# Performance work log

Measured on AMD Instinct MI355X. Metric: run time of the kernel, lower is better.

The kernel has to match this reference:

```python
import jax, jax.numpy as jnp
import numpy as np

T, B, E, H, L, V = 35, 128, 200, 512, 2, 10000


def setup_inputs() -> dict:
    key = jax.random.key(0)
    ks = jax.random.split(key, 8)
    s = 0.05  # weight init scale
    return {
        "inputs": jax.random.randint(ks[0], (T, B), 0, V),
        "hidden": jnp.zeros((L, B, H), jnp.float32),
        "emb": jax.random.normal(ks[1], (V, E), jnp.float32) * s,
        "Wx0": jax.random.normal(ks[2], (3, H, E), jnp.float32) * s,
        "Wx": jax.random.normal(ks[3], (L - 1, 3, H, H), jnp.float32) * s,
        "Wh": jax.random.normal(ks[4], (L, 3, H, H), jnp.float32) * s,
        "bh": jax.random.normal(ks[5], (L, 3, H), jnp.float32) * s,
        "Wout": jax.random.normal(ks[6], (V, H), jnp.float32) * s,
        "bout": jnp.zeros((V,), jnp.float32),
    }


def reference(inputs, hidden, emb, Wx0, Wx, Wh, bh, Wout, bout):
    # inputs: [T,B] int; hidden: [L,B,H]
    x = emb[inputs]  # [T,B,E]
    num_layers = hidden.shape[0]

    def step(h_prev, x_t):
        data = x_t  # dropout is identity (keep_prob=1.0)
        new_h = []
        for j in range(num_layers):
            Wxj = Wx0 if j == 0 else Wx[j - 1]
            gx = jnp.einsum('bi,ghi->gbh', data, Wxj)  # [3,B,H], no bias on x-side
            hp = h_prev[j]
            reset = jax.nn.sigmoid(gx[0] + hp @ Wh[j, 0].T + bh[j, 0])
            forget = jax.nn.sigmoid(gx[1] + hp @ Wh[j, 1].T + bh[j, 1])
            tild = jnp.tanh(gx[2] + (reset * hp) @ Wh[j, 2].T + bh[j, 2])
            hn = (1.0 - forget) * hp + forget * tild
            new_h.append(hn)
            data = hn  # dropout identity
        logit = data @ Wout.T + bout  # [B,V]
        return jnp.stack(new_h), logit

    h_final, logits = jax.lax.scan(step, hidden, x)
    return logits, h_final
```

## Files before the change

kernel.cpp:

```cpp
#include <hip/hip_runtime.h>
#include <hip/hip_bf16.h>

#define T_ 35
#define B_ 128
#define E_ 200
#define H_ 512
#define L_ 2
#define V_ 10000
#define BH_ (B_ * H_)
#define KPAD 224
#define NCL 4
#define CLW 48
#define NWG (NCL * CLW)

typedef __attribute__((ext_vector_type(8))) short bf16x8;
typedef __attribute__((ext_vector_type(4))) float f32x4;

__device__ __forceinline__ unsigned short f2bf(float f) {
    union { float f; unsigned u; } c; c.f = f;
    unsigned r = c.u + 0x7FFF + ((c.u >> 16) & 1);
    return (unsigned short)(r >> 16);
}
__device__ __forceinline__ float bf2f(unsigned short u) {
    union { unsigned u; float f; } c; c.u = ((unsigned)u) << 16; return c.f;
}

__device__ __forceinline__ bf16x8 cvt8(const float* src) {
    float4 w0 = *(const float4*)src;
    float4 w1 = *(const float4*)(src + 4);
    bf16x8 v;
    v[0] = (short)f2bf(w0.x); v[1] = (short)f2bf(w0.y);
    v[2] = (short)f2bf(w0.z); v[3] = (short)f2bf(w0.w);
    v[4] = (short)f2bf(w1.x); v[5] = (short)f2bf(w1.y);
    v[6] = (short)f2bf(w1.z); v[7] = (short)f2bf(w1.w);
    return v;
}

__device__ __forceinline__ void store_pair_bf16(unsigned short* buf, int idx,
                                                float v, int lane) {
    float vn = __shfl_xor(v, 1);
    if ((lane & 1) == 0) {
        unsigned p = (unsigned)f2bf(v) | ((unsigned)f2bf(vn) << 16);
        __hip_atomic_store((unsigned*)(buf + idx), p,
                           __ATOMIC_RELAXED, __HIP_MEMORY_SCOPE_AGENT);
    }
}

__global__ void prep_all(const float* __restrict__ emb, const float* __restrict__ Wx0,
                         const float* __restrict__ hidden, const float* __restrict__ Wout,
                         unsigned short* embB, unsigned short* wx0cat,
                         unsigned short* WoutB,
                         unsigned short* h0bt, unsigned short* h1bfx, int* flags) {
    int job = blockIdx.y;
    int stride = gridDim.x * blockDim.x;
    int i0 = blockIdx.x * blockDim.x + threadIdx.x;
    if (job == 0) {
        for (int i = i0; i < V_ * KPAD; i += stride) {
            int v = i / KPAD, k = i - v * KPAD;
            embB[i] = (k < E_) ? f2bf(emb[v * E_ + k]) : (unsigned short)0;
        }
    } else if (job == 1) {
        for (int i = i0; i < 1536 * KPAD; i += stride) {
            int n = i / KPAD, k = i - n * KPAD;
            wx0cat[i] = (k < E_) ? f2bf(Wx0[n * E_ + k]) : (unsigned short)0;
        }
    } else if (job == 2) {
        for (int i = i0; i < 2 * BH_; i += stride) {
            if (i < BH_) h0bt[i] = f2bf(hidden[i]);
            else         h1bfx[i - BH_] = f2bf(hidden[i]);
        }
        for (int i = i0; i < NWG * 32; i += stride) flags[i] = 0;
    } else {
        for (int i = i0; i < V_ * H_; i += stride) WoutB[i] = f2bf(Wout[i]);
    }
}

__global__ __launch_bounds__(256) void xside_gemm(
    const int* __restrict__ inputs, const unsigned short* __restrict__ embB,
    const unsigned short* __restrict__ wx0cat, float* __restrict__ gx0) {
    int m0 = blockIdx.x * 128, n0 = blockIdx.y * 128;
    int wave = threadIdx.x >> 6, lane = threadIdx.x & 63;
    int wr = wave >> 1, wc = wave & 1;
    int am = m0 + wr * 64, bn = n0 + wc * 64;
    int lr = lane & 15, lk = (lane >> 4) * 8;

    f32x4 acc[4][4] = {};
    int id[4];
    #pragma unroll
    for (int i = 0; i < 4; ++i) id[i] = inputs[am + i * 16 + lr];

    for (int k0 = 0; k0 < KPAD; k0 += 32) {
        bf16x8 a[4], b[4];
        #pragma unroll
        for (int i = 0; i < 4; ++i)
            a[i] = *(const bf16x8*)(embB + (size_t)id[i] * KPAD + k0 + lk);
        #pragma unroll
        for (int j = 0; j < 4; ++j)
            b[j] = *(const bf16x8*)(wx0cat + (size_t)(bn + j * 16 + lr) * KPAD + k0 + lk);
        #pragma unroll
        for (int i = 0; i < 4; ++i)
            #pragma unroll
            for (int j = 0; j < 4; ++j)
                acc[i][j] = __builtin_amdgcn_mfma_f32_16x16x32_bf16(a[i], b[j], acc[i][j], 0, 0, 0);
    }
    int crow0 = (lane >> 4) * 4, ccol = lane & 15;
    #pragma unroll
    for (int i = 0; i < 4; ++i) {
        #pragma unroll
        for (int r = 0; r < 4; ++r) {
            int row = am + i * 16 + crow0 + r;
            int t = row >> 7, b = row & 127;
            #pragma unroll
            for (int j = 0; j < 4; ++j) {
                int col = bn + j * 16 + ccol;
                int g = col >> 9, h = col & 511;
                gx0[((size_t)(t * 3 + g) * 128 + b) * 512 + h] = acc[i][j][r];
            }
        }
    }
}

__device__ __forceinline__ void cl_bar(int* flb, int wgl, int gen) {
    __syncthreads();
    if (threadIdx.x == 0)
        __hip_atomic_store(flb + wgl * 32, gen,
                           __ATOMIC_RELAXED, __HIP_MEMORY_SCOPE_AGENT);
    if (threadIdx.x < CLW) {
        while (__hip_atomic_load(flb + threadIdx.x * 32, __ATOMIC_RELAXED,
                                 __HIP_MEMORY_SCOPE_AGENT) < gen)
            __builtin_amdgcn_s_sleep(1);
    }
    __syncthreads();
}

__global__ __launch_bounds__(512) void scan_kernel(
    const float* __restrict__ gx0,
    const float* __restrict__ Wx, const float* __restrict__ Wh,
    const float* __restrict__ bh, const float* __restrict__ hidden,
    unsigned short* h0bt, unsigned short* rh0t, unsigned short* rh1t,
    unsigned short* h1bfx, int* flags, float* hfinal_out) {
    __shared__ unsigned short wlds[96 * 512];

    const int tid = threadIdx.x;
    const int bx = blockIdx.x;
    const int cl = bx & 3;
    const int wgl = bx >> 2;
    const int lane = tid & 63;
    const int wave = tid >> 6;
    const int lr = lane & 15;
    const int hi = lane >> 4;
    const int lk8 = hi * 8;
    const int ccol = lane & 15;
    const int crow0 = hi * 4;
    const int R0 = cl * 32;

    const bool isL0 = (wgl < 16);
    const int wid = wgl - 16;
    int* flb = flags + cl * CLW * 32;

    if (isL0) {
        for (int i = tid; i < 96 * 64; i += 512) {
            int lc = i >> 6, kg = i & 63;
            int g = lc >> 5, h = (wgl << 5) + (lc & 31);
            const float* src = Wh + (size_t)(g * 512 + h) * 512 + kg * 8;
            *(bf16x8*)(wlds + lc * 512 + (kg ^ (lc & 7)) * 8) = cvt8(src);
        }
    } else {
        for (int i = tid; i < 48 * 128; i += 512) {
            int lc = i >> 7, kg = i & 127;
            int g = lc >> 4, h = (wid << 4) + (lc & 15);
            const float* src = (kg < 64)
                ? Wx + (size_t)(g * 512 + h) * 512 + kg * 8
                : Wh + (size_t)(3 * 512 * 512) + (size_t)(g * 512 + h) * 512 + (kg - 64) * 8;
            *(bf16x8*)(wlds + lc * 1024 + (kg ^ (lc & 7)) * 8) = cvt8(src);
        }
    }

    const int mt0 = wave >> 2, nt0 = wave & 3;
    const int mt1 = (wave >> 1) & 1, nt1 = wave & 1;
    float h0reg[4], freg0[4], bias_p1_0 = 0.f, bias_p2_0 = 0.f;
    float h1reg[4], freg1[4], bias_p1_1 = 0.f, bias_p2_1 = 0.f;
    bf16x8 a0keep[16];

    if (isL0) {
        const int base = wgl << 5;
        int g = nt0 >> 1;
        int hp1 = base + (nt0 & 1) * 16 + ccol;
        bias_p1_0 = bh[g * 512 + hp1];
        if (nt0 >= 2) {
            int hc = base + (nt0 - 2) * 16 + ccol;
            int rowg = R0 + mt0 * 16;
            #pragma unroll
            for (int r = 0; r < 4; ++r)
                h0reg[r] = hidden[(size_t)(rowg + crow0 + r) * 512 + hc];
            bias_p2_0 = bh[1024 + hc];
        }
    } else {
        const int base = wid << 4;
        int hc = base + ccol;
        if (wave < 4) {
            bias_p1_1 = bh[1536 + nt1 * 512 + hc];
            if (nt1 == 1) {
                int rowg = R0 + mt1 * 16;
                #pragma unroll
                for (int r = 0; r < 4; ++r)
                    h1reg[r] = hidden[(size_t)BH_ + (size_t)(rowg + crow0 + r) * 512 + hc];
                bias_p2_1 = bh[2560 + hc];
            }
        }
    }
    __syncthreads();

    for (int s = 0; s <= 2 * T_ + 1; ++s) {
        int t = s >> 1;
        if ((s & 1) == 0) {
            if (isL0) {
                if (t < T_) {
                    const int base = wgl << 5;
                    const int rowg = R0 + mt0 * 16;
                    const unsigned short* hprev = h0bt + (size_t)t * BH_;
                    unsigned short* rh0 = rh0t + (size_t)t * BH_;
                    bf16x8 a[16];
                    #pragma unroll
                    for (int ks = 0; ks < 16; ++ks)
                        a[ks] = *(const bf16x8*)(hprev + (size_t)(rowg + lr) * 512 + ks * 32 + lk8);
                    int g = nt0 >> 1;
                    int h = base + (nt0 & 1) * 16 + ccol;
                    float gxv[4];
                    {
                        const float* gx = gx0 + (size_t)(t * 3 + g) * BH_ + h;
                        #pragma unroll
                        for (int r = 0; r < 4; ++r)
                            gxv[r] = gx[(rowg + crow0 + r) * 512];
                    }
                    f32x4 acc = {0.f, 0.f, 0.f, 0.f};
                    #pragma unroll
                    for (int ks = 0; ks < 16; ++ks) {
                        int kg = 4 * ks + hi;
                        int c = nt0 * 16 + lr;
                        bf16x8 b = *(const bf16x8*)(wlds + c * 512 + (kg ^ (c & 7)) * 8);
                        acc = __builtin_amdgcn_mfma_f32_16x16x32_bf16(a[ks], b, acc, 0, 0, 0);
                    }
                    #pragma unroll
                    for (int r = 0; r < 4; ++r) {
                        int b = rowg + crow0 + r;
                        float v = acc[r] + gxv[r] + bias_p1_0;
                        float sg = 1.f / (1.f + __expf(-v));
                        if (nt0 < 2) {
                            float h0p = bf2f(hprev[(size_t)b * 512 + h]);
                            store_pair_bf16(rh0, b * 512 + h, sg * h0p, lane);
                        } else {
                            freg0[r] = sg;
                        }
                    }
                }
            } else {
                int tc = t - 1;
                if (tc >= 0 && tc < T_ && wave < 4) {
                    const int base = wid << 4;
                    const int rowg = R0 + mt1 * 16;
                    const unsigned short* h0cur = h0bt + (size_t)(tc + 1) * BH_;
                    const unsigned short* h1prev = h1bfx + (size_t)tc * BH_;
                    unsigned short* rh1 = rh1t + (size_t)tc * BH_;
                    bf16x8 a1[16];
                    #pragma unroll
                    for (int ks = 0; ks < 16; ++ks) {
                        a0keep[ks] = *(const bf16x8*)(h0cur + (size_t)(rowg + lr) * 512 + ks * 32 + lk8);
                        a1[ks] = *(const bf16x8*)(h1prev + (size_t)(rowg + lr) * 512 + ks * 32 + lk8);
                    }
                    f32x4 acc = {0.f, 0.f, 0.f, 0.f};
                    #pragma unroll
                    for (int ks = 0; ks < 16; ++ks) {
                        int kg = 4 * ks + hi;
                        int c = nt1 * 16 + lr;
                        bf16x8 b = *(const bf16x8*)(wlds + c * 1024 + (kg ^ (c & 7)) * 8);
                        acc = __builtin_amdgcn_mfma_f32_16x16x32_bf16(a0keep[ks], b, acc, 0, 0, 0);
                    }
                    #pragma unroll
                    for (int ks = 0; ks < 16; ++ks) {
                        int kg = 64 + 4 * ks + hi;
                        int c = nt1 * 16 + lr;
                        bf16x8 b = *(const bf16x8*)(wlds + c * 1024 + (kg ^ (c & 7)) * 8);
                        acc = __builtin_amdgcn_mfma_f32_16x16x32_bf16(a1[ks], b, acc, 0, 0, 0);
                    }
                    int h = base + ccol;
                    #pragma unroll
                    for (int r = 0; r < 4; ++r) {
                        int b = rowg + crow0 + r;
                        float v = acc[r] + bias_p1_1;
                        float sg = 1.f / (1.f + __expf(-v));
                        if (nt1 == 0) {
                            float h1p = bf2f(h1prev[(size_t)b * 512 + h]);
                            store_pair_bf16(rh1, b * 512 + h, sg * h1p, lane);
                        } else {
                            freg1[r] = sg;
                        }
                    }
                }
            }
        } else {
            if (isL0) {
                if (t < T_ && nt0 >= 2) {
                    const int base = wgl << 5;
                    const int ntp = nt0 - 2;
                    const int rowg = R0 + mt0 * 16;
                    const unsigned short* rh0 = rh0t + (size_t)t * BH_;
                    unsigned short* h0nx = h0bt + (size_t)(t + 1) * BH_;
                    bf16x8 a[16];
                    #pragma unroll
                    for (int ks = 0; ks < 16; ++ks)
                        a[ks] = *(const bf16x8*)(rh0 + (size_t)(rowg + lr) * 512 + ks * 32 + lk8);
                    int h = base + ntp * 16 + ccol;
                    float gxv[4];
                    {
                        const float* gx = gx0 + (size_t)(t * 3 + 2) * BH_ + h;
                        #pragma unroll
                        for (int r = 0; r < 4; ++r)
                            gxv[r] = gx[(rowg + crow0 + r) * 512];
                    }
                    f32x4 acc = {0.f, 0.f, 0.f, 0.f};
                    #pragma unroll
                    for (int ks = 0; ks < 16; ++ks) {
                        int kg = 4 * ks + hi;
                        int c = 64 + ntp * 16 + lr;
                        bf16x8 b = *(const bf16x8*)(wlds + c * 512 + (kg ^ (c & 7)) * 8);
                        acc = __builtin_amdgcn_mfma_f32_16x16x32_bf16(a[ks], b, acc, 0, 0, 0);
                    }
                    #pragma unroll
                    for (int r = 0; r < 4; ++r) {
                        int b = rowg + crow0 + r;
                        float v = acc[r] + gxv[r] + bias_p2_0;
                        float tld = tanhf(v);
                        float hn = h0reg[r] + freg0[r] * (tld - h0reg[r]);
                        h0reg[r] = hn;
                        store_pair_bf16(h0nx, b * 512 + h, hn, lane);
                    }
                }
            } else {
                int tc = t - 1;
                if (tc >= 0 && tc < T_ && wave < 4 && nt1 == 1) {
                    const int base = wid << 4;
                    const int rowg = R0 + mt1 * 16;
                    const unsigned short* rh1 = rh1t + (size_t)tc * BH_;
                    unsigned short* h1nx = h1bfx + (size_t)(tc + 1) * BH_;
                    bf16x8 a1[16];
                    #pragma unroll
                    for (int ks = 0; ks < 16; ++ks)
                        a1[ks] = *(const bf16x8*)(rh1 + (size_t)(rowg + lr) * 512 + ks * 32 + lk8);
                    f32x4 acc = {0.f, 0.f, 0.f, 0.f};
                    #pragma unroll
                    for (int ks = 0; ks < 16; ++ks) {
                        int kg = 4 * ks + hi;
                        int c = 32 + lr;
                        bf16x8 b = *(const bf16x8*)(wlds + c * 1024 + (kg ^ (c & 7)) * 8);
                        acc = __builtin_amdgcn_mfma_f32_16x16x32_bf16(a0keep[ks], b, acc, 0, 0, 0);
                    }
                    #pragma unroll
                    for (int ks = 0; ks < 16; ++ks) {
                        int kg = 64 + 4 * ks + hi;
                        int c = 32 + lr;
                        bf16x8 b = *(const bf16x8*)(wlds + c * 1024 + (kg ^ (c & 7)) * 8);
                        acc = __builtin_amdgcn_mfma_f32_16x16x32_bf16(a1[ks], b, acc, 0, 0, 0);
                    }
                    int h = base + ccol;
                    #pragma unroll
                    for (int r = 0; r < 4; ++r) {
                        int b = rowg + crow0 + r;
                        float v = acc[r] + bias_p2_1;
                        float tld = tanhf(v);
                        float hn = h1reg[r] + freg1[r] * (tld - h1reg[r]);
                        h1reg[r] = hn;
                        store_pair_bf16(h1nx, b * 512 + h, hn, lane);
                    }
                }
            }
        }
        cl_bar(flb, wgl, s + 1);
    }

    if (isL0) {
        if (nt0 >= 2) {
            const int base = wgl << 5;
            int hc = base + (nt0 - 2) * 16 + ccol;
            int rowg = R0 + mt0 * 16;
            #pragma unroll
            for (int r = 0; r < 4; ++r)
                hfinal_out[(size_t)(rowg + crow0 + r) * 512 + hc] = h0reg[r];
        }
    } else if (wave < 4 && nt1 == 1) {
        const int base = wid << 4;
        int rowg = R0 + mt1 * 16;
        #pragma unroll
        for (int r = 0; r < 4; ++r)
            hfinal_out[(size_t)BH_ + (size_t)(rowg + crow0 + r) * 512 + base + ccol] = h1reg[r];
    }
}

#define MT_ (T_ * B_ / 128)
#define NT_ ((V_ + 127) / 128)
__global__ __launch_bounds__(256) void logits_gemm(
    const unsigned short* __restrict__ A, const unsigned short* __restrict__ Bw,
    const float* __restrict__ bout, float* __restrict__ C) {
    const int nwg = MT_ * NT_;
    const int q = nwg / 8, rr = nwg % 8;
    int bid = blockIdx.x;
    int xcd = bid % 8, idx = bid / 8;
    int wgid = (xcd < rr ? xcd * (q + 1) : rr * (q + 1) + (xcd - rr) * q) + idx;
    int n0 = (wgid / MT_) * 128;
    int m0 = (wgid % MT_) * 128;

    int wave = threadIdx.x >> 6, lane = threadIdx.x & 63;
    int wr = wave >> 1, wc = wave & 1;
    int am = m0 + wr * 64, bn = n0 + wc * 64;
    int lr = lane & 15, lk = (lane >> 4) * 8;

    f32x4 acc[4][4] = {};
    bf16x8 a[4], b[4], an[4], bnx[4];
    #pragma unroll
    for (int i = 0; i < 4; ++i)
        a[i] = *(const bf16x8*)(A + (size_t)(am + i * 16 + lr) * H_ + lk);
    #pragma unroll
    for (int j = 0; j < 4; ++j) {
        int colc = bn + j * 16 + lr; if (colc >= V_) colc = V_ - 1;
        b[j] = *(const bf16x8*)(Bw + (size_t)colc * H_ + lk);
    }
    for (int k0 = 0; k0 < H_; k0 += 32) {
        if (k0 + 32 < H_) {
            #pragma unroll
            for (int i = 0; i < 4; ++i)
                an[i] = *(const bf16x8*)(A + (size_t)(am + i * 16 + lr) * H_ + k0 + 32 + lk);
            #pragma unroll
            for (int j = 0; j < 4; ++j) {
                int colc = bn + j * 16 + lr; if (colc >= V_) colc = V_ - 1;
                bnx[j] = *(const bf16x8*)(Bw + (size_t)colc * H_ + k0 + 32 + lk);
            }
        }
        #pragma unroll
        for (int i = 0; i < 4; ++i)
            #pragma unroll
            for (int j = 0; j < 4; ++j)
                acc[i][j] = __builtin_amdgcn_mfma_f32_16x16x32_bf16(a[i], b[j], acc[i][j], 0, 0, 0);
        #pragma unroll
        for (int i = 0; i < 4; ++i) { a[i] = an[i]; b[i] = bnx[i]; }
    }
    int crow0 = (lane >> 4) * 4, ccol = lane & 15;
    #pragma unroll
    for (int j = 0; j < 4; ++j) {
        int col = bn + j * 16 + ccol;
        if (col >= V_) continue;
        float bv = bout[col];
        #pragma unroll
        for (int i = 0; i < 4; ++i) {
            #pragma unroll
            for (int r = 0; r < 4; ++r) {
                int row = am + i * 16 + crow0 + r;
                __builtin_nontemporal_store(acc[i][j][r] + bv, &C[(size_t)row * V_ + col]);
            }
        }
    }
}

extern "C" void kernel_launch(void* const* d_in, const int* in_sizes, int n_in,
                              void* d_out, int out_size, void* d_ws, size_t ws_size,
                              hipStream_t stream) {
    const int*   inputs = (const int*)  d_in[0];
    const float* hidden = (const float*)d_in[1];
    const float* emb    = (const float*)d_in[2];
    const float* Wx0    = (const float*)d_in[3];
    const float* Wx     = (const float*)d_in[4];
    const float* Wh     = (const float*)d_in[5];
    const float* bh     = (const float*)d_in[6];
    const float* Wout   = (const float*)d_in[7];
    const float* bout   = (const float*)d_in[8];
    float* out = (float*)d_out;
    (void)in_sizes; (void)n_in; (void)out_size; (void)ws_size;

    char* ws = (char*)d_ws;
    size_t off = 0;
    auto alloc = [&](size_t bytes) -> void* {
        void* p = ws + off;
        off += (bytes + 255) & ~(size_t)255;
        return p;
    };
    unsigned short* embB   = (unsigned short*)alloc((size_t)V_ * KPAD * 2);
    unsigned short* wx0cat = (unsigned short*)alloc((size_t)1536 * KPAD * 2);
    unsigned short* WoutB  = (unsigned short*)alloc((size_t)V_ * H_ * 2);
    unsigned short* h1bfx  = (unsigned short*)alloc((size_t)(T_ + 1) * BH_ * 2);
    int* flags = (int*)alloc(NWG * 32 * 4);

    float* gx0 = out;
    unsigned short* scr = (unsigned short*)(out + (size_t)T_ * 3 * BH_);
    unsigned short* h0bt = scr;
    unsigned short* rh0t = scr + (size_t)(T_ + 1) * BH_;
    unsigned short* rh1t = scr + (size_t)(2 * T_ + 1) * BH_;

    prep_all<<<dim3(1024, 4), dim3(256), 0, stream>>>(
        emb, Wx0, hidden, Wout, embB, wx0cat, WoutB, h0bt, h1bfx, flags);
    xside_gemm<<<dim3(T_, 12), dim3(256), 0, stream>>>(inputs, embB, wx0cat, gx0);
    scan_kernel<<<dim3(NWG), dim3(512), 0, stream>>>(
        gx0, Wx, Wh, bh, hidden,
        h0bt, rh0t, rh1t, h1bfx, flags,
        out + (size_t)T_ * B_ * V_);
    logits_gemm<<<dim3(MT_ * NT_), dim3(256), 0, stream>>>(
        h1bfx + BH_, WoutB, bout, out);
}
```

Measured before the change: 653.0 us.

## Split cluster barrier into separate layer-0 and layer-1 barriers with dependency flags

Replaces the single 48-workgroup cluster barrier with separate barriers for layer-0 (16 WGs) and layer-1 (32 WGs). Layer-1 waits only on the layer-0 progress flags it depends on, so layer 0 can run ahead and the two layers are no longer in lockstep. MFMA accumulation is also split into two independent accumulator chains to shorten dependency latency. The risk is relaxed ordering on the flag protocol and layer 0 racing ahead. Correctness depends on the flag generations matching.

```diff
diff --git a/kernel.cpp b/kernel.cpp
--- a/kernel.cpp
+++ b/kernel.cpp
@@ -120,14 +120,31 @@
     }
 }
 
-__device__ __forceinline__ void cl_bar(int* flb, int wgl, int gen) {
+__device__ __forceinline__ void bar_l0(int* flb, int wgl, int gen) {
     __syncthreads();
     if (threadIdx.x == 0)
         __hip_atomic_store(flb + wgl * 32, gen,
                            __ATOMIC_RELAXED, __HIP_MEMORY_SCOPE_AGENT);
-    if (threadIdx.x < CLW) {
+    if (threadIdx.x < 16) {
         while (__hip_atomic_load(flb + threadIdx.x * 32, __ATOMIC_RELAXED,
                                  __HIP_MEMORY_SCOPE_AGENT) < gen)
+            __builtin_amdgcn_s_sleep(1);
+    }
+    __syncthreads();
+}
+
+__device__ __forceinline__ void bar_l1(int* flb, int wid, int gen, int l0need) {
+    __syncthreads();
+    if (threadIdx.x == 0)
+        __hip_atomic_store(flb + (16 + wid) * 32, gen,
+                           __ATOMIC_RELAXED, __HIP_MEMORY_SCOPE_AGENT);
+    if (threadIdx.x < 32) {
+        while (__hip_atomic_load(flb + (16 + threadIdx.x) * 32, __ATOMIC_RELAXED,
+                                 __HIP_MEMORY_SCOPE_AGENT) < gen)
+            __builtin_amdgcn_s_sleep(1);
+    } else if (threadIdx.x < 48) {
+        while (__hip_atomic_load(flb + (threadIdx.x - 32) * 32, __ATOMIC_RELAXED,
+                                 __HIP_MEMORY_SCOPE_AGENT) < l0need)
             __builtin_amdgcn_s_sleep(1);
     }
     __syncthreads();
@@ -211,52 +228,108 @@
     }
     __syncthreads();
 
-    for (int s = 0; s <= 2 * T_ + 1; ++s) {
-        int t = s >> 1;
-        if ((s & 1) == 0) {
-            if (isL0) {
-                if (t < T_) {
-                    const int base = wgl << 5;
-                    const int rowg = R0 + mt0 * 16;
-                    const unsigned short* hprev = h0bt + (size_t)t * BH_;
-                    unsigned short* rh0 = rh0t + (size_t)t * BH_;
-                    bf16x8 a[16];
-                    #pragma unroll
-                    for (int ks = 0; ks < 16; ++ks)
-                        a[ks] = *(const bf16x8*)(hprev + (size_t)(rowg + lr) * 512 + ks * 32 + lk8);
-                    int g = nt0 >> 1;
-                    int h = base + (nt0 & 1) * 16 + ccol;
-                    float gxv[4];
-                    {
-                        const float* gx = gx0 + (size_t)(t * 3 + g) * BH_ + h;
-                        #pragma unroll
-                        for (int r = 0; r < 4; ++r)
-                            gxv[r] = gx[(rowg + crow0 + r) * 512];
-                    }
-                    f32x4 acc = {0.f, 0.f, 0.f, 0.f};
-                    #pragma unroll
-                    for (int ks = 0; ks < 16; ++ks) {
-                        int kg = 4 * ks + hi;
-                        int c = nt0 * 16 + lr;
-                        bf16x8 b = *(const bf16x8*)(wlds + c * 512 + (kg ^ (c & 7)) * 8);
-                        acc = __builtin_amdgcn_mfma_f32_16x16x32_bf16(a[ks], b, acc, 0, 0, 0);
-                    }
-                    #pragma unroll
-                    for (int r = 0; r < 4; ++r) {
-                        int b = rowg + crow0 + r;
-                        float v = acc[r] + gxv[r] + bias_p1_0;
-                        float sg = 1.f / (1.f + __expf(-v));
-                        if (nt0 < 2) {
-                            float h0p = bf2f(hprev[(size_t)b * 512 + h]);
-                            store_pair_bf16(rh0, b * 512 + h, sg * h0p, lane);
-                        } else {
-                            freg0[r] = sg;
-                        }
-                    }
-                }
-            } else {
-                int tc = t - 1;
-                if (tc >= 0 && tc < T_ && wave < 4) {
+    if (isL0) {
+        for (int s = 0; s < 2 * T_; ++s) {
+            bar_l0(flb, wgl, s);
+            int t = s >> 1;
+            if ((s & 1) == 0) {
+                const int base = wgl << 5;
+                const int rowg = R0 + mt0 * 16;
+                const unsigned short* hprev = h0bt + (size_t)t * BH_;
+                unsigned short* rh0 = rh0t + (size_t)t * BH_;
+                bf16x8 a[16];
+                #pragma unroll
+                for (int ks = 0; ks < 16; ++ks)
+                    a[ks] = *(const bf16x8*)(hprev + (size_t)(rowg + lr) * 512 + ks * 32 + lk8);
+                int g = nt0 >> 1;
+                int h = base + (nt0 & 1) * 16 + ccol;
+                float gxv[4];
+                {
+                    const float* gx = gx0 + (size_t)(t * 3 + g) * BH_ + h;
+                    #pragma unroll
+                    for (int r = 0; r < 4; ++r)
+                        gxv[r] = gx[(rowg + crow0 + r) * 512];
+                }
+                f32x4 accA = {0.f, 0.f, 0.f, 0.f}, accB = {0.f, 0.f, 0.f, 0.f};
+                #pragma unroll
+                for (int ks = 0; ks < 16; ks += 2) {
+                    int c = nt0 * 16 + lr;
+                    int kgA = 4 * ks + hi, kgB = 4 * (ks + 1) + hi;
+                    bf16x8 bA = *(const bf16x8*)(wlds + c * 512 + (kgA ^ (c & 7)) * 8);
+                    bf16x8 bB = *(const bf16x8*)(wlds + c * 512 + (kgB ^ (c & 7)) * 8);
+                    accA = __builtin_amdgcn_mfma_f32_16x16x32_bf16(a[ks], bA, accA, 0, 0, 0);
+                    accB = __builtin_amdgcn_mfma_f32_16x16x32_bf16(a[ks + 1], bB, accB, 0, 0, 0);
+                }
+                #pragma unroll
+                for (int r = 0; r < 4; ++r) {
+                    int b = rowg + crow0 + r;
+                    float v = accA[r] + accB[r] + gxv[r] + bias_p1_0;
+                    float sg = 1.f / (1.f + __expf(-v));
+                    if (nt0 < 2) {
+                        float h0p = bf2f(hprev[(size_t)b * 512 + h]);
+                        store_pair_bf16(rh0, b * 512 + h, sg * h0p, lane);
+                    } else {
+                        freg0[r] = sg;
+                    }
+                }
+            } else if (nt0 >= 2) {
+                const int base = wgl << 5;
+                const int ntp = nt0 - 2;
+                const int rowg = R0 + mt0 * 16;
+                const unsigned short* rh0 = rh0t + (size_t)t * BH_;
+                unsigned short* h0nx = h0bt + (size_t)(t + 1) * BH_;
+                bf16x8 a[16];
+                #pragma unroll
+                for (int ks = 0; ks < 16; ++ks)
+                    a[ks] = *(const bf16x8*)(rh0 + (size_t)(rowg + lr) * 512 + ks * 32 + lk8);
+                int h = base + ntp * 16 + ccol;
+                float gxv[4];
+                {
+                    const float* gx = gx0 + (size_t)(t * 3 + 2) * BH_ + h;
+                    #pragma unroll
+                    for (int r = 0; r < 4; ++r)
+                        gxv[r] = gx[(rowg + crow0 + r) * 512];
+                }
+                f32x4 accA = {0.f, 0.f, 0.f, 0.f}, accB = {0.f, 0.f, 0.f, 0.f};
+                #pragma unroll
+                for (int ks = 0; ks < 16; ks += 2) {
+                    int c = 64 + ntp * 16 + lr;
+                    int kgA = 4 * ks + hi, kgB = 4 * (ks + 1) + hi;
+                    bf16x8 bA = *(const bf16x8*)(wlds + c * 512 + (kgA ^ (c & 7)) * 8);
+                    bf16x8 bB = *(const bf16x8*)(wlds + c * 512 + (kgB ^ (c & 7)) * 8);
+                    accA = __builtin_amdgcn_mfma_f32_16x16x32_bf16(a[ks], bA, accA, 0, 0, 0);
+                    accB = __builtin_amdgcn_mfma_f32_16x16x32_bf16(a[ks + 1], bB, accB, 0, 0, 0);
+                }
+                #pragma unroll
+                for (int r = 0; r < 4; ++r) {
+                    int b = rowg + crow0 + r;
+                    float v = accA[r] + accB[r] + gxv[r] + bias_p2_0;
+                    float tld = tanhf(v);
+                    float hn = h0reg[r] + freg0[r] * (tld - h0reg[r]);
+                    h0reg[r] = hn;
+                    store_pair_bf16(h0nx, b * 512 + h, hn, lane);
+                }
+            }
+        }
+        __syncthreads();
+        if (tid == 0)
+            __hip_atomic_store(flb + wgl * 32, 2 * T_,
+                               __ATOMIC_RELAXED, __HIP_MEMORY_SCOPE_AGENT);
+        if (nt0 >= 2) {
+            const int base = wgl << 5;
+            int hc = base + (nt0 - 2) * 16 + ccol;
+            int rowg = R0 + mt0 * 16;
+            #pragma unroll
+            for (int r = 0; r < 4; ++r)
+                hfinal_out[(size_t)(rowg + crow0 + r) * 512 + hc] = h0reg[r];
+        }
+    } else {
+        for (int s = 0; s < 2 * T_; ++s) {
+            int tc = s >> 1;
+            int l0need = ((s & 1) == 0) ? (2 * tc + 2) : 0;
+            bar_l1(flb, wid, s, l0need);
+            if ((s & 1) == 0) {
+                if (wave < 4) {
                     const int base = wid << 4;
                     const int rowg = R0 + mt1 * 16;
                     const unsigned short* h0cur = h0bt + (size_t)(tc + 1) * BH_;
@@ -268,26 +341,26 @@
                         a0keep[ks] = *(const bf16x8*)(h0cur + (size_t)(rowg + lr) * 512 + ks * 32 + lk8);
                         a1[ks] = *(const bf16x8*)(h1prev + (size_t)(rowg + lr) * 512 + ks * 32 + lk8);
                     }
-                    f32x4 acc = {0.f, 0.f, 0.f, 0.f};
+                    f32x4 accA = {0.f, 0.f, 0.f, 0.f}, accB = {0.f, 0.f, 0.f, 0.f};
                     #pragma unroll
                     for (int ks = 0; ks < 16; ++ks) {
                         int kg = 4 * ks + hi;
                         int c = nt1 * 16 + lr;
                         bf16x8 b = *(const bf16x8*)(wlds + c * 1024 + (kg ^ (c & 7)) * 8);
-                        acc = __builtin_amdgcn_mfma_f32_16x16x32_bf16(a0keep[ks], b, acc, 0, 0, 0);
+                        accA = __builtin_amdgcn_mfma_f32_16x16x32_bf16(a0keep[ks], b, accA, 0, 0, 0);
                     }
                     #pragma unroll
                     for (int ks = 0; ks < 16; ++ks) {
                         int kg = 64 + 4 * ks + hi;
                         int c = nt1 * 16 + lr;
                         bf16x8 b = *(const bf16x8*)(wlds + c * 1024 + (kg ^ (c & 7)) * 8);
-                        acc = __builtin_amdgcn_mfma_f32_16x16x32_bf16(a1[ks], b, acc, 0, 0, 0);
+                        accB = __builtin_amdgcn_mfma_f32_16x16x32_bf16(a1[ks], b, accB, 0, 0, 0);
                     }
                     int h = base + ccol;
                     #pragma unroll
                     for (int r = 0; r < 4; ++r) {
                         int b = rowg + crow0 + r;
-                        float v = acc[r] + bias_p1_1;
+                        float v = accA[r] + accB[r] + bias_p1_1;
                         float sg = 1.f / (1.f + __expf(-v));
                         if (nt1 == 0) {
                             float h1p = bf2f(h1prev[(size_t)b * 512 + h]);
@@ -297,48 +370,8 @@
                         }
                     }
                 }
-            }
-        } else {
-            if (isL0) {
-                if (t < T_ && nt0 >= 2) {
-                    const int base = wgl << 5;
-                    const int ntp = nt0 - 2;
-                    const int rowg = R0 + mt0 * 16;
-                    const unsigned short* rh0 = rh0t + (size_t)t * BH_;
-                    unsigned short* h0nx = h0bt + (size_t)(t + 1) * BH_;
-                    bf16x8 a[16];
-                    #pragma unroll
-                    for (int ks = 0; ks < 16; ++ks)
-                        a[ks] = *(const bf16x8*)(rh0 + (size_t)(rowg + lr) * 512 + ks * 32 + lk8);
-                    int h = base + ntp * 16 + ccol;
-                    float gxv[4];
-                    {
-                        const float* gx = gx0 + (size_t)(t * 3 + 2) * BH_ + h;
-                        #pragma unroll
-                        for (int r = 0; r < 4; ++r)
-                            gxv[r] = gx[(rowg + crow0 + r) * 512];
-                    }
-                    f32x4 acc = {0.f, 0.f, 0.f, 0.f};
-                    #pragma unroll
-                    for (int ks = 0; ks < 16; ++ks) {
-                        int kg = 4 * ks + hi;
-                        int c = 64 + ntp * 16 + lr;
-                        bf16x8 b = *(const bf16x8*)(wlds + c * 512 + (kg ^ (c & 7)) * 8);
-                        acc = __builtin_amdgcn_mfma_f32_16x16x32_bf16(a[ks], b, acc, 0, 0, 0);
-                    }
-                    #pragma unroll
-                    for (int r = 0; r < 4; ++r) {
-                        int b = rowg + crow0 + r;
-                        float v = acc[r] + gxv[r] + bias_p2_0;
-                        float tld = tanhf(v);
-                        float hn = h0reg[r] + freg0[r] * (tld - h0reg[r]);
-                        h0reg[r] = hn;
-                        store_pair_bf16(h0nx, b * 512 + h, hn, lane);
-                    }
-                }
             } else {
-                int tc = t - 1;
-                if (tc >= 0 && tc < T_ && wave < 4 && nt1 == 1) {
+                if (wave < 4 && nt1 == 1) {
                     const int base = wid << 4;
                     const int rowg = R0 + mt1 * 16;
                     const unsigned short* rh1 = rh1t + (size_t)tc * BH_;
@@ -347,26 +380,26 @@
                     #pragma unroll
                     for (int ks = 0; ks < 16; ++ks)
                         a1[ks] = *(const bf16x8*)(rh1 + (size_t)(rowg + lr) * 512 + ks * 32 + lk8);
-                    f32x4 acc = {0.f, 0.f, 0.f, 0.f};
+                    f32x4 accA = {0.f, 0.f, 0.f, 0.f}, accB = {0.f, 0.f, 0.f, 0.f};
                     #pragma unroll
                     for (int ks = 0; ks < 16; ++ks) {
                         int kg = 4 * ks + hi;
                         int c = 32 + lr;
                         bf16x8 b = *(const bf16x8*)(wlds + c * 1024 + (kg ^ (c & 7)) * 8);
-                        acc = __builtin_amdgcn_mfma_f32_16x16x32_bf16(a0keep[ks], b, acc, 0, 0, 0);
+                        accA = __builtin_amdgcn_mfma_f32_16x16x32_bf16(a0keep[ks], b, accA, 0, 0, 0);
                     }
                     #pragma unroll
                     for (int ks = 0; ks < 16; ++ks) {
                         int kg = 64 + 4 * ks + hi;
                         int c = 32 + lr;
                         bf16x8 b = *(const bf16x8*)(wlds + c * 1024 + (kg ^ (c & 7)) * 8);
-                        acc = __builtin_amdgcn_mfma_f32_16x16x32_bf16(a1[ks], b, acc, 0, 0, 0);
+                        accB = __builtin_amdgcn_mfma_f32_16x16x32_bf16(a1[ks], b, accB, 0, 0, 0);
                     }
                     int h = base + ccol;
                     #pragma unroll
                     for (int r = 0; r < 4; ++r) {
                         int b = rowg + crow0 + r;
-                        float v = acc[r] + bias_p2_1;
+                        float v = accA[r] + accB[r] + bias_p2_1;
                         float tld = tanhf(v);
                         float hn = h1reg[r] + freg1[r] * (tld - h1reg[r]);
                         h1reg[r] = hn;
@@ -375,24 +408,13 @@
                 }
             }
         }
-        cl_bar(flb, wgl, s + 1);
-    }
-
-    if (isL0) {
-        if (nt0 >= 2) {
-            const int base = wgl << 5;
-            int hc = base + (nt0 - 2) * 16 + ccol;
-            int rowg = R0 + mt0 * 16;
+        if (wave < 4 && nt1 == 1) {
+            const int base = wid << 4;
+            int rowg = R0 + mt1 * 16;
             #pragma unroll
             for (int r = 0; r < 4; ++r)
-                hfinal_out[(size_t)(rowg + crow0 + r) * 512 + hc] = h0reg[r];
-        }
-    } else if (wave < 4 && nt1 == 1) {
-        const int base = wid << 4;
-        int rowg = R0 + mt1 * 16;
-        #pragma unroll
-        for (int r = 0; r < 4; ++r)
-            hfinal_out[(size_t)BH_ + (size_t)(rowg + crow0 + r) * 512 + base + ccol] = h1reg[r];
+                hfinal_out[(size_t)BH_ + (size_t)(rowg + crow0 + r) * 512 + base + ccol] = h1reg[r];
+        }
     }
 }
 
```

New measurement: 602.6 us. -7.7%, faster.

## Decouple GRU layer workgroups with per-phase counters and split-K across all waves

Applied to the files above, without the earlier changes.

Replaces the lockstep per-cluster flag barrier, where all 48 workgroups wait for each other every phase, with separate per-phase atomic counters for layer 0 and layer 1. Layer 1 now polls only the layer-0 counter it depends on, so the two layers pipeline rather than run in a fixed skewed lockstep. It also splits the K dimension of the candidate and layer-1 matmuls across otherwise idle waves, reducing partial sums through LDS, so all 8 waves do work and each wave's serial MFMA chain is shorter. The cost is extra __syncthreads and LDS traffic per phase and a larger counter array. Layer 0 may also run ahead of layer 1 with no backpressure, which depends on every timestep keeping its own buffers.

```diff
diff --git a/kernel.cpp b/kernel.cpp
--- a/kernel.cpp
+++ b/kernel.cpp
@@ -12,6 +12,7 @@
 #define NCL 4
 #define CLW 48
 #define NWG (NCL * CLW)
+#define NPH 80
 
 typedef __attribute__((ext_vector_type(8))) short bf16x8;
 typedef __attribute__((ext_vector_type(4))) float f32x4;
@@ -50,7 +51,7 @@
                          const float* __restrict__ hidden, const float* __restrict__ Wout,
                          unsigned short* embB, unsigned short* wx0cat,
                          unsigned short* WoutB,
-                         unsigned short* h0bt, unsigned short* h1bfx, int* flags) {
+                         unsigned short* h0bt, unsigned short* h1bfx, int* cnt) {
     int job = blockIdx.y;
     int stride = gridDim.x * blockDim.x;
     int i0 = blockIdx.x * blockDim.x + threadIdx.x;
@@ -69,7 +70,7 @@
             if (i < BH_) h0bt[i] = f2bf(hidden[i]);
             else         h1bfx[i - BH_] = f2bf(hidden[i]);
         }
-        for (int i = i0; i < NWG * 32; i += stride) flags[i] = 0;
+        for (int i = i0; i < NCL * 2 * NPH * 32; i += stride) cnt[i] = 0;
     } else {
         for (int i = i0; i < V_ * H_; i += stride) WoutB[i] = f2bf(Wout[i]);
     }
@@ -120,14 +121,11 @@
     }
 }
 
-__device__ __forceinline__ void cl_bar(int* flb, int wgl, int gen) {
+__device__ __forceinline__ void bar_cnt(int* c, int n) {
     __syncthreads();
-    if (threadIdx.x == 0)
-        __hip_atomic_store(flb + wgl * 32, gen,
-                           __ATOMIC_RELAXED, __HIP_MEMORY_SCOPE_AGENT);
-    if (threadIdx.x < CLW) {
-        while (__hip_atomic_load(flb + threadIdx.x * 32, __ATOMIC_RELAXED,
-                                 __HIP_MEMORY_SCOPE_AGENT) < gen)
+    if (threadIdx.x == 0) {
+        __hip_atomic_fetch_add(c, 1, __ATOMIC_RELAXED, __HIP_MEMORY_SCOPE_AGENT);
+        while (__hip_atomic_load(c, __ATOMIC_RELAXED, __HIP_MEMORY_SCOPE_AGENT) < n)
             __builtin_amdgcn_s_sleep(1);
     }
     __syncthreads();
@@ -138,8 +136,9 @@
     const float* __restrict__ Wx, const float* __restrict__ Wh,
     const float* __restrict__ bh, const float* __restrict__ hidden,
     unsigned short* h0bt, unsigned short* rh0t, unsigned short* rh1t,
-    unsigned short* h1bfx, int* flags, float* hfinal_out) {
+    unsigned short* h1bfx, int* cnt, float* hfinal_out) {
     __shared__ unsigned short wlds[96 * 512];
+    __shared__ f32x4 psum[4][64];
 
     const int tid = threadIdx.x;
     const int bx = blockIdx.x;
@@ -156,7 +155,8 @@
 
     const bool isL0 = (wgl < 16);
     const int wid = wgl - 16;
-    int* flb = flags + cl * CLW * 32;
+    int* cnt_l0 = cnt + (cl * 2 + 0) * NPH * 32;
+    int* cnt_l1 = cnt + (cl * 2 + 1) * NPH * 32;
 
     if (isL0) {
         for (int i = tid; i < 96 * 64; i += 512) {
@@ -177,7 +177,7 @@
     }
 
     const int mt0 = wave >> 2, nt0 = wave & 3;
-    const int mt1 = (wave >> 1) & 1, nt1 = wave & 1;
+    const int m1 = (wave >> 2) & 1, n1 = (wave >> 1) & 1, kh1 = wave & 1;
     float h0reg[4], freg0[4], bias_p1_0 = 0.f, bias_p2_0 = 0.f;
     float h1reg[4], freg1[4], bias_p1_1 = 0.f, bias_p2_1 = 0.f;
     bf16x8 a0keep[16];
@@ -198,118 +198,83 @@
     } else {
         const int base = wid << 4;
         int hc = base + ccol;
-        if (wave < 4) {
-            bias_p1_1 = bh[1536 + nt1 * 512 + hc];
-            if (nt1 == 1) {
-                int rowg = R0 + mt1 * 16;
+        if (kh1 == 0) bias_p1_1 = bh[1536 + n1 * 512 + hc];
+        if (kh1 == 0 && n1 == 1) {
+            int rowg = R0 + m1 * 16;
+            #pragma unroll
+            for (int r = 0; r < 4; ++r)
+                h1reg[r] = hidden[(size_t)BH_ + (size_t)(rowg + crow0 + r) * 512 + hc];
+            bias_p2_1 = bh[2560 + hc];
+        }
+    }
+    __syncthreads();
+
+    if (isL0) {
+        for (int s = 0; s < 2 * T_; ++s) {
+            int t = s >> 1;
+            if ((s & 1) == 0) {
+                const int base = wgl << 5;
+                const int rowg = R0 + mt0 * 16;
+                const unsigned short* hprev = h0bt + (size_t)t * BH_;
+                unsigned short* rh0 = rh0t + (size_t)t * BH_;
+                bf16x8 a[16];
                 #pragma unroll
-                for (int r = 0; r < 4; ++r)
-                    h1reg[r] = hidden[(size_t)BH_ + (size_t)(rowg + crow0 + r) * 512 + hc];
-                bias_p2_1 = bh[2560 + hc];
-            }
-        }
-    }
-    __syncthreads();
-
-    for (int s = 0; s <= 2 * T_ + 1; ++s) {
-        int t = s >> 1;
-        if ((s & 1) == 0) {
-            if (isL0) {
-                if (t < T_) {
-                    const int base = wgl << 5;
-                    const int rowg = R0 + mt0 * 16;
-                    const unsigned short* hprev = h0bt + (size_t)t * BH_;
-                    unsigned short* rh0 = rh0t + (size_t)t * BH_;
-                    bf16x8 a[16];
-                    #pragma unroll
-                    for (int ks = 0; ks < 16; ++ks)
-                        a[ks] = *(const bf16x8*)(hprev + (size_t)(rowg + lr) * 512 + ks * 32 + lk8);
-                    int g = nt0 >> 1;
-                    int h = base + (nt0 & 1) * 16 + ccol;
-                    float gxv[4];
-                    {
-                        const float* gx = gx0 + (size_t)(t * 3 + g) * BH_ + h;
-                        #pragma unroll
-                        for (int r = 0; r < 4; ++r)
-                            gxv[r] = gx[(rowg + crow0 + r) * 512];
-                    }
-                    f32x4 acc = {0.f, 0.f, 0.f, 0.f};
-                    #pragma unroll
-                    for (int ks = 0; ks < 16; ++ks) {
-                        int kg = 4 * ks + hi;
-                        int c = nt0 * 16 + lr;
-                        bf16x8 b = *(const bf16x8*)(wlds + c * 512 + (kg ^ (c & 7)) * 8);
-                        acc = __builtin_amdgcn_mfma_f32_16x16x32_bf16(a[ks], b, acc, 0, 0, 0);
-                    }
-                    #pragma unroll
-                    for (int r = 0; r < 4; ++r) {
-                        int b = rowg + crow0 + r;
-                        float v = acc[r] + gxv[r] + bias_p1_0;
-                        float sg = 1.f / (1.f + __expf(-v));
-                        if (nt0 < 2) {
-                            float h0p = bf2f(hprev[(size_t)b * 512 + h]);
-                            store_pair_bf16(rh0, b * 512 + h, sg * h0p, lane);
-                        } else {
-                            freg0[r] = sg;
-                        }
+                for (int ks = 0; ks < 16; ++ks)
+                    a[ks] = *(const bf16x8*)(hprev + (size_t)(rowg + lr) * 512 + ks * 32 + lk8);
+                int g = nt0 >> 1;
+                int h = base + (nt0 & 1) * 16 + ccol;
+                float gxv[4];
+                {
+                    const float* gx = gx0 + (size_t)(t * 3 + g) * BH_ + h;
+                    #pragma unroll
+                    for (int r = 0; r < 4; ++r)
+                        gxv[r] = gx[(rowg + crow0 + r) * 512];
+                }
+                f32x4 accA = {0.f, 0.f, 0.f, 0.f}, accB = {0.f, 0.f, 0.f, 0.f};
+                #pragma unroll
+                for (int ks = 0; ks < 16; ks += 2) {
+                    int c = nt0 * 16 + lr;
+                    int kgA = 4 * ks + hi, kgB = 4 * (ks + 1) + hi;
+                    bf16x8 bA = *(const bf16x8*)(wlds + c * 512 + (kgA ^ (c & 7)) * 8);
+                    bf16x8 bB = *(const bf16x8*)(wlds + c * 512 + (kgB ^ (c & 7)) * 8);
+                    accA = __builtin_amdgcn_mfma_f32_16x16x32_bf16(a[ks], bA, accA, 0, 0, 0);
+                    accB = __builtin_amdgcn_mfma_f32_16x16x32_bf16(a[ks + 1], bB, accB, 0, 0, 0);
+                }
+                #pragma unroll
+                for (int r = 0; r < 4; ++r) {
+                    int b = rowg + crow0 + r;
+                    float v = accA[r] + accB[r] + gxv[r] + bias_p1_0;
+                    float sg = 1.f / (1.f + __expf(-v));
+                    if (nt0 < 2) {
+                        float h0p = bf2f(hprev[(size_t)b * 512 + h]);
+                        store_pair_bf16(rh0, b * 512 + h, sg * h0p, lane);
+                    } else {
+                        freg0[r] = sg;
                     }
                 }
             } else {
-                int tc = t - 1;
-                if (tc >= 0 && tc < T_ && wave < 4) {
-                    const int base = wid << 4;
-                    const int rowg = R0 + mt1 * 16;
-                    const unsigned short* h0cur = h0bt + (size_t)(tc + 1) * BH_;
-                    const unsigned short* h1prev = h1bfx + (size_t)tc * BH_;
-                    unsigned short* rh1 = rh1t + (size_t)tc * BH_;
-                    bf16x8 a1[16];
-                    #pragma unroll
-                    for (int ks = 0; ks < 16; ++ks) {
-                        a0keep[ks] = *(const bf16x8*)(h0cur + (size_t)(rowg + lr) * 512 + ks * 32 + lk8);
-                        a1[ks] = *(const bf16x8*)(h1prev + (size_t)(rowg + lr) * 512 + ks * 32 + lk8);
-                    }
-                    f32x4 acc = {0.f, 0.f, 0.f, 0.f};
-                    #pragma unroll
-                    for (int ks = 0; ks < 16; ++ks) {
-                        int kg = 4 * ks + hi;
-                        int c = nt1 * 16 + lr;
-                        bf16x8 b = *(const bf16x8*)(wlds + c * 1024 + (kg ^ (c & 7)) * 8);
-                        acc = __builtin_amdgcn_mfma_f32_16x16x32_bf16(a0keep[ks], b, acc, 0, 0, 0);
-                    }
-                    #pragma unroll
-                    for (int ks = 0; ks < 16; ++ks) {
-                        int kg = 64 + 4 * ks + hi;
-                        int c = nt1 * 16 + lr;
-                        bf16x8 b = *(const bf16x8*)(wlds + c * 1024 + (kg ^ (c & 7)) * 8);
-                        acc = __builtin_amdgcn_mfma_f32_16x16x32_bf16(a1[ks], b, acc, 0, 0, 0);
-                    }
-                    int h = base + ccol;
-                    #pragma unroll
-                    for (int r = 0; r < 4; ++r) {
-                        int b = rowg + crow0 + r;
-                        float v = acc[r] + bias_p1_1;
-                        float sg = 1.f / (1.f + __expf(-v));
-                        if (nt1 == 0) {
-                            float h1p = bf2f(h1prev[(size_t)b * 512 + h]);
-                            store_pair_bf16(rh1, b * 512 + h, sg * h1p, lane);
-                        } else {
-                            freg1[r] = sg;
-                        }
-                    }
-                }
-            }
-        } else {
-            if (isL0) {
-                if (t < T_ && nt0 >= 2) {
-                    const int base = wgl << 5;
-                    const int ntp = nt0 - 2;
-                    const int rowg = R0 + mt0 * 16;
-                    const unsigned short* rh0 = rh0t + (size_t)t * BH_;
-                    unsigned short* h0nx = h0bt + (size_t)(t + 1) * BH_;
-                    bf16x8 a[16];
-                    #pragma unroll
-                    for (int ks = 0; ks < 16; ++ks)
-                        a[ks] = *(const bf16x8*)(rh0 + (size_t)(rowg + lr) * 512 + ks * 32 + lk8);
+                const int base = wgl << 5;
+                const int ntp = (nt0 >= 2) ? (nt0 - 2) : nt0;
+                const int ksb = (nt0 >= 2) ? 0 : 8;
+                const int rowg = R0 + mt0 * 16;
+                const unsigned short* rh0 = rh0t + (size_t)t * BH_;
+                unsigned short* h0nx = h0bt + (size_t)(t + 1) * BH_;
+                bf16x8 a[8];
+                #pragma unroll
+                for (int ks = 0; ks < 8; ++ks)
+                    a[ks] = *(const bf16x8*)(rh0 + (size_t)(rowg + lr) * 512 + (ksb + ks) * 32 + lk8);
+                f32x4 acc = {0.f, 0.f, 0.f, 0.f};
+                #pragma unroll
+                for (int ks = 0; ks < 8; ++ks) {
+                    int c = 64 + ntp * 16 + lr;
+                    int kg = 4 * (ksb + ks) + hi;
+                    bf16x8 b = *(const bf16x8*)(wlds + c * 512 + (kg ^ (c & 7)) * 8);
+                    acc = __builtin_amdgcn_mfma_f32_16x16x32_bf16(a[ks], b, acc, 0, 0, 0);
+                }
+                if (nt0 < 2) psum[mt0 * 2 + ntp][lane] = acc;
+                __syncthreads();
+                if (nt0 >= 2) {
+                    f32x4 p = psum[mt0 * 2 + ntp][lane];
                     int h = base + ntp * 16 + ccol;
                     float gxv[4];
                     {
@@ -318,55 +283,124 @@
                         for (int r = 0; r < 4; ++r)
                             gxv[r] = gx[(rowg + crow0 + r) * 512];
                     }
-                    f32x4 acc = {0.f, 0.f, 0.f, 0.f};
-                    #pragma unroll
-                    for (int ks = 0; ks < 16; ++ks) {
-                        int kg = 4 * ks + hi;
-                        int c = 64 + ntp * 16 + lr;
-                        bf16x8 b = *(const bf16x8*)(wlds + c * 512 + (kg ^ (c & 7)) * 8);
-                        acc = __builtin_amdgcn_mfma_f32_16x16x32_bf16(a[ks], b, acc, 0, 0, 0);
-                    }
                     #pragma unroll
                     for (int r = 0; r < 4; ++r) {
                         int b = rowg + crow0 + r;
-                        float v = acc[r] + gxv[r] + bias_p2_0;
+                        float v = acc[r] + p[r] + gxv[r] + bias_p2_0;
                         float tld = tanhf(v);
                         float hn = h0reg[r] + freg0[r] * (tld - h0reg[r]);
                         h0reg[r] = hn;
                         store_pair_bf16(h0nx, b * 512 + h, hn, lane);
                     }
                 }
-            } else {
-                int tc = t - 1;
-                if (tc >= 0 && tc < T_ && wave < 4 && nt1 == 1) {
-                    const int base = wid << 4;
-                    const int rowg = R0 + mt1 * 16;
-                    const unsigned short* rh1 = rh1t + (size_t)tc * BH_;
-                    unsigned short* h1nx = h1bfx + (size_t)(tc + 1) * BH_;
-                    bf16x8 a1[16];
+            }
+            bar_cnt(cnt_l0 + s * 32, 16);
+        }
+        if (nt0 >= 2) {
+            const int base = wgl << 5;
+            int hc = base + (nt0 - 2) * 16 + ccol;
+            int rowg = R0 + mt0 * 16;
+            #pragma unroll
+            for (int r = 0; r < 4; ++r)
+                hfinal_out[(size_t)(rowg + crow0 + r) * 512 + hc] = h0reg[r];
+        }
+    } else {
+        for (int s = 0; s < 2 * T_; ++s) {
+            int tc = s >> 1;
+            if ((s & 1) == 0) {
+                if (tid == 0) {
+                    int* lc = cnt_l0 + (2 * tc + 1) * 32;
+                    while (__hip_atomic_load(lc, __ATOMIC_RELAXED,
+                                             __HIP_MEMORY_SCOPE_AGENT) < 16)
+                        __builtin_amdgcn_s_sleep(1);
+                }
+                __syncthreads();
+                const int base = wid << 4;
+                const int rowg = R0 + m1 * 16;
+                const unsigned short* h0cur = h0bt + (size_t)(tc + 1) * BH_;
+                const unsigned short* h1prev = h1bfx + (size_t)tc * BH_;
+                unsigned short* rh1 = rh1t + (size_t)tc * BH_;
+                f32x4 acc = {0.f, 0.f, 0.f, 0.f};
+                if (kh1 == 0) {
                     #pragma unroll
                     for (int ks = 0; ks < 16; ++ks)
-                        a1[ks] = *(const bf16x8*)(rh1 + (size_t)(rowg + lr) * 512 + ks * 32 + lk8);
-                    f32x4 acc = {0.f, 0.f, 0.f, 0.f};
+                        a0keep[ks] = *(const bf16x8*)(h0cur + (size_t)(rowg + lr) * 512 + ks * 32 + lk8);
                     #pragma unroll
                     for (int ks = 0; ks < 16; ++ks) {
                         int kg = 4 * ks + hi;
-                        int c = 32 + lr;
+                        int c = n1 * 16 + lr;
                         bf16x8 b = *(const bf16x8*)(wlds + c * 1024 + (kg ^ (c & 7)) * 8);
                         acc = __builtin_amdgcn_mfma_f32_16x16x32_bf16(a0keep[ks], b, acc, 0, 0, 0);
                     }
+                } else {
+                    bf16x8 a1[16];
+                    #pragma unroll
+                    for (int ks = 0; ks < 16; ++ks)
+                        a1[ks] = *(const bf16x8*)(h1prev + (size_t)(rowg + lr) * 512 + ks * 32 + lk8);
                     #pragma unroll
                     for (int ks = 0; ks < 16; ++ks) {
                         int kg = 64 + 4 * ks + hi;
-                        int c = 32 + lr;
+                        int c = n1 * 16 + lr;
                         bf16x8 b = *(const bf16x8*)(wlds + c * 1024 + (kg ^ (c & 7)) * 8);
                         acc = __builtin_amdgcn_mfma_f32_16x16x32_bf16(a1[ks], b, acc, 0, 0, 0);
                     }
+                    psum[m1 * 2 + n1][lane] = acc;
+                }
+                __syncthreads();
+                if (kh1 == 0) {
+                    f32x4 p = psum[m1 * 2 + n1][lane];
                     int h = base + ccol;
                     #pragma unroll
                     for (int r = 0; r < 4; ++r) {
                         int b = rowg + crow0 + r;
-                        float v = acc[r] + bias_p2_1;
+                        float v = acc[r] + p[r] + bias_p1_1;
+                        float sg = 1.f / (1.f + __expf(-v));
+                        if (n1 == 0) {
+                            float h1p = bf2f(h1prev[(size_t)b * 512 + h]);
+                            store_pair_bf16(rh1, b * 512 + h, sg * h1p, lane);
+                        } else {
+                            freg1[r] = sg;
+                        }
+                    }
+                }
+            } else {
+                const int base = wid << 4;
+                const int rowg = R0 + m1 * 16;
+                const unsigned short* rh1 = rh1t + (size_t)tc * BH_;
+                unsigned short* h1nx = h1bfx + (size_t)(tc + 1) * BH_;
+                f32x4 acc = {0.f, 0.f, 0.f, 0.f};
+                if (n1 == 1) {
+                    if (kh1 == 0) {
+                        #pragma unroll
+                        for (int ks = 0; ks < 16; ++ks) {
+                            int kg = 4 * ks + hi;
+                            int c = 32 + lr;
+                            bf16x8 b = *(const bf16x8*)(wlds + c * 1024 + (kg ^ (c & 7)) * 8);
+                            acc = __builtin_amdgcn_mfma_f32_16x16x32_bf16(a0keep[ks], b, acc, 0, 0, 0);
+                        }
+                    } else {
+                        bf16x8 a1[16];
+                        #pragma unroll
+                        for (int ks = 0; ks < 16; ++ks)
+                            a1[ks] = *(const bf16x8*)(rh1 + (size_t)(rowg + lr) * 512 + ks * 32 + lk8);
+                        #pragma unroll
+                        for (int ks = 0; ks < 16; ++ks) {
+                            int kg = 64 + 4 * ks + hi;
+                            int c = 32 + lr;
+                            bf16x8 b = *(const bf16x8*)(wlds + c * 1024 + (kg ^ (c & 7)) * 8);
+                            acc = __builtin_amdgcn_mfma_f32_16x16x32_bf16(a1[ks], b, acc, 0, 0, 0);
+                        }
+                        psum[m1][lane] = acc;
+                    }
+                }
+                __syncthreads();
+                if (n1 == 1 && kh1 == 0) {
+                    f32x4 p = psum[m1][lane];
+                    int h = base + ccol;
+                    #pragma unroll
+                    for (int r = 0; r < 4; ++r) {
+                        int b = rowg + crow0 + r;
+                        float v = acc[r] + p[r] + bias_p2_1;
                         float tld = tanhf(v);
                         float hn = h1reg[r] + freg1[r] * (tld - h1reg[r]);
                         h1reg[r] = hn;
@@ -374,25 +408,15 @@
                     }
                 }
             }
-        }
-        cl_bar(flb, wgl, s + 1);
-    }
-
-    if (isL0) {
-        if (nt0 >= 2) {
-            const int base = wgl << 5;
-            int hc = base + (nt0 - 2) * 16 + ccol;
-            int rowg = R0 + mt0 * 16;
+            bar_cnt(cnt_l1 + s * 32, 32);
+        }
+        if (kh1 == 0 && n1 == 1) {
+            const int base = wid << 4;
+            int rowg = R0 + m1 * 16;
             #pragma unroll
             for (int r = 0; r < 4; ++r)
-                hfinal_out[(size_t)(rowg + crow0 + r) * 512 + hc] = h0reg[r];
-        }
-    } else if (wave < 4 && nt1 == 1) {
-        const int base = wid << 4;
-        int rowg = R0 + mt1 * 16;
-        #pragma unroll
-        for (int r = 0; r < 4; ++r)
-            hfinal_out[(size_t)BH_ + (size_t)(rowg + crow0 + r) * 512 + base + ccol] = h1reg[r];
+                hfinal_out[(size_t)BH_ + (size_t)(rowg + crow0 + r) * 512 + base + ccol] = h1reg[r];
+        }
     }
 }
 
@@ -486,7 +510,7 @@
     unsigned short* wx0cat = (unsigned short*)alloc((size_t)1536 * KPAD * 2);
     unsigned short* WoutB  = (unsigned short*)alloc((size_t)V_ * H_ * 2);
     unsigned short* h1bfx  = (unsigned short*)alloc((size_t)(T_ + 1) * BH_ * 2);
-    int* flags = (int*)alloc(NWG * 32 * 4);
+    int* cnt = (int*)alloc((size_t)NCL * 2 * NPH * 32 * 4);
 
     float* gx0 = out;
     unsigned short* scr = (unsigned short*)(out + (size_t)T_ * 3 * BH_);
@@ -495,11 +519,11 @@
     unsigned short* rh1t = scr + (size_t)(2 * T_ + 1) * BH_;
 
     prep_all<<<dim3(1024, 4), dim3(256), 0, stream>>>(
-        emb, Wx0, hidden, Wout, embB, wx0cat, WoutB, h0bt, h1bfx, flags);
+        emb, Wx0, hidden, Wout, embB, wx0cat, WoutB, h0bt, h1bfx, cnt);
     xside_gemm<<<dim3(T_, 12), dim3(256), 0, stream>>>(inputs, embB, wx0cat, gx0);
     scan_kernel<<<dim3(NWG), dim3(512), 0, stream>>>(
         gx0, Wx, Wh, bh, hidden,
-        h0bt, rh0t, rh1t, h1bfx, flags,
+        h0bt, rh0t, rh1t, h1bfx, cnt,
         out + (size_t)T_ * B_ * V_);
     logits_gemm<<<dim3(MT_ * NT_), dim3(256), 0, stream>>>(
         h1bfx + BH_, WoutB, bout, out);
```

Result: faster. 638.2 us (-2.3%).
